# Optimization experiments

Hardware: AMD Instinct MI355X
Metric: run time of the kernel (lower is better)

Reference implementation:

```python
import jax, jax.numpy as jnp
import numpy as np

D_MODEL = 1024
NUM_HEADS = 16
D_K = D_MODEL // NUM_HEADS


def setup_inputs() -> dict:
    key = jax.random.key(0)
    ks = jax.random.split(key, 9)
    s = 1.0 / np.sqrt(D_MODEL)
    x = jax.random.normal(ks[0], (2, 2048, D_MODEL), dtype=jnp.float32)
    Wq = jax.random.uniform(ks[1], (D_MODEL, D_MODEL), jnp.float32, -s, s)
    bq = jax.random.uniform(ks[2], (D_MODEL,), jnp.float32, -s, s)
    Wk = jax.random.uniform(ks[3], (D_MODEL, D_MODEL), jnp.float32, -s, s)
    bk = jax.random.uniform(ks[4], (D_MODEL,), jnp.float32, -s, s)
    Wv = jax.random.uniform(ks[5], (D_MODEL, D_MODEL), jnp.float32, -s, s)
    bv = jax.random.uniform(ks[6], (D_MODEL,), jnp.float32, -s, s)
    Wo = jax.random.uniform(ks[7], (D_MODEL, D_MODEL), jnp.float32, -s, s)
    bo = jax.random.uniform(ks[8], (D_MODEL,), jnp.float32, -s, s)
    return {"x": x, "Wq": Wq, "bq": bq, "Wk": Wk, "bk": bk,
            "Wv": Wv, "bv": bv, "Wo": Wo, "bo": bo}


def reference(x, Wq, bq, Wk, bk, Wv, bv, Wo, bo):
    B, S, _ = x.shape
    # torch Linear: y = x @ W.T + b
    def proj(W, b):
        h = x @ W.T + b                       # [B,S,D]
        return h.reshape(B, S, NUM_HEADS, D_K).transpose(0, 2, 1, 3)  # [B,H,S,Dk]
    Q = proj(Wq, bq)
    K = proj(Wk, bk)
    V = proj(Wv, bv)
    scale = 1.0 / np.sqrt(D_K)
    scores = jnp.einsum('bhqd,bhkd->bhqk', Q, K) * scale   # [B,H,S,S]
    causal = jnp.triu(jnp.ones((S, S), dtype=bool), k=1)   # True above diag
    scores = jnp.where(causal, -jnp.inf, scores)
    probs = jax.nn.softmax(scores, axis=-1)
    out = jnp.einsum('bhqk,bhkd->bhqd', probs, V)          # [B,H,S,Dk]
    out = out.transpose(0, 2, 1, 3).reshape(B, S, NUM_HEADS * D_K)
    return out @ Wo.T + bo
```

## Files before the change

kernel.cpp:

```cpp
#include <hip/hip_runtime.h>

typedef unsigned short u16;
typedef __attribute__((ext_vector_type(8))) short short8;
typedef __attribute__((ext_vector_type(4))) float floatx4;

__device__ __forceinline__ u16 f2bf(float x){
  union { float f; unsigned u; } v; v.f = x;
  unsigned r = v.u + 0x7fffu + ((v.u >> 16) & 1u);
  return (u16)(r >> 16);
}

__device__ __forceinline__ unsigned cvt_pk_bf16(float lo, float hi){
  unsigned r;
  asm("v_cvt_pk_bf16_f32 %0, %1, %2" : "=v"(r) : "v"(lo), "v"(hi));
  return r;
}

__device__ __forceinline__ float exp2_raw(float x){
  float r;
  asm("v_exp_f32 %0, %1" : "=v"(r) : "v"(x));
  return r;
}

__device__ __forceinline__ void gld16(const u16* g, u16* l){
  __builtin_amdgcn_global_load_lds(
      (const __attribute__((address_space(1))) void*)g,
      (__attribute__((address_space(3))) void*)l, 16, 0, 0);
}

#define WAIT_BAR_V4() asm volatile("s_waitcnt vmcnt(4) lgkmcnt(0)\ns_barrier" ::: "memory")
#define WAIT_BAR_V3() asm volatile("s_waitcnt vmcnt(3) lgkmcnt(0)\ns_barrier" ::: "memory")
#define WAIT_BAR_V0() asm volatile("s_waitcnt vmcnt(0) lgkmcnt(0)\ns_barrier" ::: "memory")

__global__ void k_cvt_all(const float* __restrict__ x,
                          const float* __restrict__ wq, const float* __restrict__ wk,
                          const float* __restrict__ wv, const float* __restrict__ wo,
                          u16* __restrict__ xb, u16* __restrict__ wqb, u16* __restrict__ wkb,
                          u16* __restrict__ wvb, u16* __restrict__ wob){
  const int i = blockIdx.x * 256 + threadIdx.x;
  const float* s; u16* d; int off;
  if (i < 1048576) { s = x; d = xb; off = i; }
  else {
    const int j = i - 1048576;
    const int wsel = j >> 18;
    off = j & 262143;
    s = (wsel==0) ? wq : (wsel==1) ? wk : (wsel==2) ? wv : wo;
    d = (wsel==0) ? wqb : (wsel==1) ? wkb : (wsel==2) ? wvb : wob;
  }
  const float4 f = ((const float4*)s)[off];
  unsigned lo = (unsigned)f2bf(f.x) | ((unsigned)f2bf(f.y) << 16);
  unsigned hi = (unsigned)f2bf(f.z) | ((unsigned)f2bf(f.w) << 16);
  ((uint2*)d)[off] = make_uint2(lo, hi);
}

__global__ __launch_bounds__(256) void k_gemm_qkv(
    const u16* __restrict__ A,
    const u16* __restrict__ Wq, const u16* __restrict__ Wk, const u16* __restrict__ Wv,
    const float* __restrict__ bq, const float* __restrict__ bk, const float* __restrict__ bv,
    u16* __restrict__ Qo, u16* __restrict__ Ko, u16* __restrict__ Vo)
{
  const int bid = (int)blockIdx.x;
  const int xcd = bid & 7;
  const int i5  = bid >> 3;
  const int xb_ = ((xcd >> 2) << 2) + (i5 & 3);
  const int rest = i5 >> 2;
  const int yb_ = ((xcd & 3) << 3) + (rest & 7);
  const int mode = rest >> 3;

  const u16* W      = (mode==1) ? Wk : (mode==2) ? Wv : Wq;
  const float* bias = (mode==1) ? bk : (mode==2) ? bv : bq;

  __shared__ u16 lA[3][4096];
  __shared__ u16 lB[3][4096];

  const int tid  = threadIdx.x;
  const int row0 = yb_ * 128;
  const int col0 = xb_ * 128;

  const int srow = tid >> 2;
  const int sgp  = tid & 3;
  const int sgl  = sgp ^ ((srow >> 1) & 3);
  const u16* ga0 = A + (row0 + srow)      * 1024 + sgl * 8;
  const u16* ga1 = A + (row0 + srow + 64) * 1024 + sgl * 8;
  const u16* gb0 = W + (col0 + srow)      * 1024 + sgl * 8;
  const u16* gb1 = W + (col0 + srow + 64) * 1024 + sgl * 8;

  const int l  = tid & 63, w = tid >> 6;
  const int wr = w >> 1,  wc = w & 1;
  const int lr = l & 15,  grp = l >> 4;
  const int sw = (lr >> 1) & 3;
  int aoff[4], boff[4];
#pragma unroll
  for (int m = 0; m < 4; ++m) aoff[m] = (wr*64 + m*16 + lr)*32 + ((grp ^ sw) * 8);
#pragma unroll
  for (int n = 0; n < 4; ++n) boff[n] = (wc*64 + n*16 + lr)*32 + ((grp ^ sw) * 8);

  floatx4 acc[4][4];
#pragma unroll
  for (int m = 0; m < 4; ++m)
#pragma unroll
    for (int n = 0; n < 4; ++n) acc[m][n] = (floatx4){0.f, 0.f, 0.f, 0.f};

#define STAGE(buf, kt_) do { \
    const int k0_ = (kt_) * 32; \
    gld16(ga0 + k0_, &lA[(buf)][tid*8]); \
    gld16(ga1 + k0_, &lA[(buf)][2048 + tid*8]); \
    gld16(gb0 + k0_, &lB[(buf)][tid*8]); \
    gld16(gb1 + k0_, &lB[(buf)][2048 + tid*8]); \
  } while (0)

  STAGE(0, 0);
  STAGE(1, 1);
  asm volatile("s_waitcnt vmcnt(4)\ns_barrier" ::: "memory");

  for (int kt0 = 0; kt0 < 32; kt0 += 3) {
#pragma unroll
    for (int i = 0; i < 3; ++i) {
      const int kt = kt0 + i;
      if (kt >= 32) break;
      const bool st2 = (kt + 2 < 32);
      if (st2) STAGE((i + 2) % 3, kt + 2);
      short8 af[4], bf[4];
#pragma unroll
      for (int m = 0; m < 4; ++m) af[m] = *(const short8*)&lA[i][aoff[m]];
#pragma unroll
      for (int n = 0; n < 4; ++n) bf[n] = *(const short8*)&lB[i][boff[n]];
#pragma unroll
      for (int m = 0; m < 4; ++m)
#pragma unroll
        for (int n = 0; n < 4; ++n)
          acc[m][n] = __builtin_amdgcn_mfma_f32_16x16x32_bf16(af[m], bf[n], acc[m][n], 0, 0, 0);
      if (st2) WAIT_BAR_V4(); else WAIT_BAR_V0();
    }
  }
#undef STAGE

  const float sc = (mode == 0) ? 0.18033688011112042f : 1.0f;
  u16* dst = (mode == 0) ? Qo : (mode == 1) ? Ko : Vo;
#pragma unroll
  for (int n = 0; n < 4; ++n) {
    const int cg = col0 + wc*64 + n*16 + lr;
    const float bb = bias[cg];
    const int h = cg >> 6, d = cg & 63;
#pragma unroll
    for (int m = 0; m < 4; ++m) {
#pragma unroll
      for (int j = 0; j < 4; ++j) {
        const int rg = row0 + wr*64 + m*16 + grp*4 + j;
        const int b = rg >> 11, s5 = rg & 2047;
        const float val = (acc[m][n][j] + bb) * sc;
        int idx;
        if (mode == 2) idx = ((b*16 + h)*64 + d)*2048 + s5;
        else           idx = ((b*16 + h)*2048 + s5)*64 + d;
        dst[idx] = f2bf(val);
      }
    }
  }
}

__global__ __launch_bounds__(256) void k_gemm_o(
    const u16* __restrict__ A, const u16* __restrict__ W,
    const float* __restrict__ bias, float* __restrict__ Fo)
{
  const int bid = (int)blockIdx.x;
  const int xcd = bid & 7;
  const int i5  = bid >> 3;
  const int xb_ = ((xcd >> 2) << 2) + (i5 & 3);
  const int yb_ = ((xcd & 3) << 4) + (i5 >> 2);

  __shared__ u16 lA[3][2048];
  __shared__ u16 lB[3][4096];

  const int tid  = threadIdx.x;
  const int row0 = yb_ * 64;
  const int col0 = xb_ * 128;

  const int srow = tid >> 2;
  const int sgp  = tid & 3;
  const int sgl  = sgp ^ ((srow >> 1) & 3);
  const u16* ga0 = A + (row0 + srow)      * 1024 + sgl * 8;
  const u16* gb0 = W + (col0 + srow)      * 1024 + sgl * 8;
  const u16* gb1 = W + (col0 + srow + 64) * 1024 + sgl * 8;

  const int l  = tid & 63, w = tid >> 6;
  const int wr = w >> 1,  wc = w & 1;
  const int lr = l & 15,  grp = l >> 4;
  const int sw = (lr >> 1) & 3;
  int aoff[2], boff[4];
#pragma unroll
  for (int m = 0; m < 2; ++m) aoff[m] = (wr*32 + m*16 + lr)*32 + ((grp ^ sw) * 8);
#pragma unroll
  for (int n = 0; n < 4; ++n) boff[n] = (wc*64 + n*16 + lr)*32 + ((grp ^ sw) * 8);

  floatx4 acc[2][4];
#pragma unroll
  for (int m = 0; m < 2; ++m)
#pragma unroll
    for (int n = 0; n < 4; ++n) acc[m][n] = (floatx4){0.f, 0.f, 0.f, 0.f};

#define STAGE(buf, kt_) do { \
    const int k0_ = (kt_) * 32; \
    gld16(ga0 + k0_, &lA[(buf)][tid*8]); \
    gld16(gb0 + k0_, &lB[(buf)][tid*8]); \
    gld16(gb1 + k0_, &lB[(buf)][2048 + tid*8]); \
  } while (0)

  STAGE(0, 0);
  STAGE(1, 1);
  asm volatile("s_waitcnt vmcnt(3)\ns_barrier" ::: "memory");

  for (int kt0 = 0; kt0 < 32; kt0 += 3) {
#pragma unroll
    for (int i = 0; i < 3; ++i) {
      const int kt = kt0 + i;
      if (kt >= 32) break;
      const bool st2 = (kt + 2 < 32);
      if (st2) STAGE((i + 2) % 3, kt + 2);
      short8 af[2], bf[4];
#pragma unroll
      for (int m = 0; m < 2; ++m) af[m] = *(const short8*)&lA[i][aoff[m]];
#pragma unroll
      for (int n = 0; n < 4; ++n) bf[n] = *(const short8*)&lB[i][boff[n]];
#pragma unroll
      for (int m = 0; m < 2; ++m)
#pragma unroll
        for (int n = 0; n < 4; ++n)
          acc[m][n] = __builtin_amdgcn_mfma_f32_16x16x32_bf16(af[m], bf[n], acc[m][n], 0, 0, 0);
      if (st2) WAIT_BAR_V3(); else WAIT_BAR_V0();
    }
  }
#undef STAGE

#pragma unroll
  for (int n = 0; n < 4; ++n) {
    const int cg = col0 + wc*64 + n*16 + lr;
    const float bb = bias[cg];
#pragma unroll
    for (int m = 0; m < 2; ++m) {
      const int rg = row0 + wr*32 + m*16 + grp*4;
#pragma unroll
      for (int j = 0; j < 4; ++j)
        Fo[(rg + j) * 1024 + cg] = acc[m][n][j] + bb;
    }
  }
}

__global__ __launch_bounds__(256, 4) void k_attn(
    const u16* __restrict__ Q, const u16* __restrict__ K,
    const u16* __restrict__ V, u16* __restrict__ O)
{
  __shared__ u16 lK[2][4096];
  __shared__ u16 lV[2][4096];
  __shared__ u16 lP[4][1024];

  const int tid = threadIdx.x;
  const int bid = (int)blockIdx.x;
  const int xcd = bid & 7, r = bid >> 3;
  const int k_ = r & 31, j_ = r >> 5;
  const int bh = xcd * 4 + j_;
  const int qt = (j_ & 1) ? k_ : (31 - k_);

  const int l = tid & 63, w = tid >> 6;
  const int lr = l & 15, grp = l >> 4;
  const int qw0 = qt * 64 + w * 16;
  const int nkt = qt + 1;

  const u16* Qh = Q + (size_t)bh * 2048 * 64;
  const u16* Kh = K + (size_t)bh * 2048 * 64;
  const u16* Vh = V + (size_t)bh * 64 * 2048;

  const int srow = tid >> 3, sgp = tid & 7;
  const int sgl = sgp ^ (srow & 7);
  u16* lPw = &lP[w][0];
  const int swz = lr & 7;
  const int b = bh >> 4, h = bh & 15;

#define STAGEKV(buf, kt_) do { \
    gld16(Kh + ((kt_)*64 + srow     )*64 + sgl*8, &lK[(buf)][tid*8]); \
    gld16(Kh + ((kt_)*64 + srow + 32)*64 + sgl*8, &lK[(buf)][2048 + tid*8]); \
    gld16(Vh + (srow     )*2048 + (kt_)*64 + sgl*8, &lV[(buf)][tid*8]); \
    gld16(Vh + (srow + 32)*2048 + (kt_)*64 + sgl*8, &lV[(buf)][2048 + tid*8]); \
  } while (0)

  short8 qf[2];
#pragma unroll
  for (int kk = 0; kk < 2; ++kk)
    qf[kk] = *(const short8*)(Qh + (qw0 + lr)*64 + kk*32 + grp*8);

  floatx4 accO[4];
  float mrow = -1e30f, lrow = 0.f;
#pragma unroll
  for (int dn = 0; dn < 4; ++dn) accO[dn] = (floatx4){0.f, 0.f, 0.f, 0.f};

  STAGEKV(0, 0);
  __syncthreads();

  for (int kt0 = 0; kt0 < nkt; kt0 += 2) {
#pragma unroll
    for (int i = 0; i < 2; ++i) {
      const int kt = kt0 + i;
      if (kt >= nkt) break;
      if (kt + 1 < nkt) STAGEKV(i ^ 1, kt + 1);
      const int kb = kt * 64;

      floatx4 st[4];
#pragma unroll
      for (int n = 0; n < 4; ++n) st[n] = (floatx4){0.f, 0.f, 0.f, 0.f};
#pragma unroll
      for (int n = 0; n < 4; ++n) {
        const int key = n*16 + lr;
#pragma unroll
        for (int kk = 0; kk < 2; ++kk) {
          const int gp = (kk*4 + grp) ^ (key & 7);
          short8 kf = *(const short8*)&lK[i][key*64 + gp*8];
          st[n] = __builtin_amdgcn_mfma_f32_16x16x32_bf16(kf, qf[kk], st[n], 0, 0, 0);
        }
      }

      const int lim = qw0 + lr - kb;
      if (63 > lim) {
#pragma unroll
        for (int n = 0; n < 4; ++n)
#pragma unroll
          for (int jj = 0; jj < 4; ++jj)
            if (n*16 + grp*4 + jj > lim) st[n][jj] = -1e30f;
      }

      float mt = st[0][0];
#pragma unroll
      for (int n = 0; n < 4; ++n)
#pragma unroll
        for (int jj = 0; jj < 4; ++jj) mt = fmaxf(mt, st[n][jj]);
      if (!__all(mt <= mrow + 8.0f)) {
        float mg = fmaxf(mt, __shfl_xor(mt, 16));
        mg = fmaxf(mg, __shfl_xor(mg, 32));
        const float mn = fmaxf(mrow, mg);
        const float alpha = exp2_raw(mrow - mn);
        mrow = mn;
        lrow *= alpha;
#pragma unroll
        for (int dn = 0; dn < 4; ++dn) accO[dn] *= alpha;
      }
      float ps = 0.f;
#pragma unroll
      for (int n = 0; n < 4; ++n)
#pragma unroll
        for (int jj = 0; jj < 4; ++jj) {
          const float p = exp2_raw(st[n][jj] - mrow);
          st[n][jj] = p;
          ps += p;
        }
      lrow += ps;

#pragma unroll
      for (int n = 0; n < 4; ++n)
#pragma unroll
        for (int p2 = 0; p2 < 2; ++p2) {
          const unsigned pk = cvt_pk_bf16(st[n][2*p2], st[n][2*p2+1]);
          const int pg = (2*n + (grp >> 1)) ^ swz;
          ((unsigned*)lPw)[lr*32 + pg*4 + (grp & 1)*2 + p2] = pk;
        }

      asm volatile("s_waitcnt lgkmcnt(0)" ::: "memory");

      short8 pa[2];
#pragma unroll
      for (int kk = 0; kk < 2; ++kk)
        pa[kk] = *(const short8*)&lPw[lr*64 + (((kk*4 + grp) ^ swz) * 8)];

#pragma unroll
      for (int dn = 0; dn < 4; ++dn) {
        const int d = dn*16 + lr;
#pragma unroll
        for (int kk = 0; kk < 2; ++kk) {
          const int gp = (kk*4 + grp) ^ (d & 7);
          short8 vf = *(const short8*)&lV[i][d*64 + gp*8];
          accO[dn] = __builtin_amdgcn_mfma_f32_16x16x32_bf16(vf, pa[kk], accO[dn], 0, 0, 0);
        }
      }
      __syncthreads();
    }
  }

  float lt = lrow + __shfl_xor(lrow, 16);
  lt += __shfl_xor(lt, 32);
  const float inv = 1.0f / lt;
  const int token = b*2048 + qw0 + lr;
#pragma unroll
  for (int dn = 0; dn < 4; ++dn)
#pragma unroll
    for (int p2 = 0; p2 < 2; ++p2) {
      const unsigned pk = cvt_pk_bf16(accO[dn][2*p2] * inv, accO[dn][2*p2+1] * inv);
      *(unsigned*)&O[token*1024 + h*64 + dn*16 + grp*4 + 2*p2] = pk;
    }
#undef STAGEKV
}

extern "C" void kernel_launch(void* const* d_in, const int* in_sizes, int n_in,
                              void* d_out, int out_size, void* d_ws, size_t ws_size,
                              hipStream_t stream) {
  const float* x  = (const float*)d_in[0];
  const float* Wq = (const float*)d_in[1];
  const float* bq = (const float*)d_in[2];
  const float* Wk = (const float*)d_in[3];
  const float* bk = (const float*)d_in[4];
  const float* Wv = (const float*)d_in[5];
  const float* bv = (const float*)d_in[6];
  const float* Wo = (const float*)d_in[7];
  const float* bo = (const float*)d_in[8];
  float* out = (float*)d_out;

  char* ws = (char*)d_ws;
  u16* xb  = (u16*)(ws + 0);
  u16* wqb = (u16*)(ws + 8388608);
  u16* wkb = (u16*)(ws + 10485760);
  u16* wvb = (u16*)(ws + 12582912);
  u16* wob = (u16*)(ws + 14680064);
  u16* Qb  = (u16*)(ws + 16777216);
  u16* Kb  = (u16*)(ws + 25165824);
  u16* Vb  = (u16*)(ws + 33554432);
  u16* Ab  = (u16*)(ws + 41943040);

  k_cvt_all<<<dim3(8192), 256, 0, stream>>>(x, Wq, Wk, Wv, Wo, xb, wqb, wkb, wvb, wob);

  k_gemm_qkv<<<dim3(768), 256, 0, stream>>>(xb, wqb, wkb, wvb, bq, bk, bv, Qb, Kb, Vb);

  k_attn<<<dim3(1024), 256, 0, stream>>>(Qb, Kb, Vb, Ab);

  k_gemm_o<<<dim3(512), 256, 0, stream>>>(Ab, wob, bo, out);
}
```

Baseline: 106.3 us.

## Fuse Q/K/V projections into one block sharing the A tile

```diff
diff --git a/kernel.cpp b/kernel.cpp
--- a/kernel.cpp
+++ b/kernel.cpp
@@ -28,7 +28,6 @@
       (__attribute__((address_space(3))) void*)l, 16, 0, 0);
 }
 
-#define WAIT_BAR_V4() asm volatile("s_waitcnt vmcnt(4) lgkmcnt(0)\ns_barrier" ::: "memory")
 #define WAIT_BAR_V3() asm volatile("s_waitcnt vmcnt(3) lgkmcnt(0)\ns_barrier" ::: "memory")
 #define WAIT_BAR_V0() asm volatile("s_waitcnt vmcnt(0) lgkmcnt(0)\ns_barrier" ::: "memory")
 
@@ -63,15 +62,10 @@
   const int xcd = bid & 7;
   const int i5  = bid >> 3;
   const int xb_ = ((xcd >> 2) << 2) + (i5 & 3);
-  const int rest = i5 >> 2;
-  const int yb_ = ((xcd & 3) << 3) + (rest & 7);
-  const int mode = rest >> 3;
-
-  const u16* W      = (mode==1) ? Wk : (mode==2) ? Wv : Wq;
-  const float* bias = (mode==1) ? bk : (mode==2) ? bv : bq;
-
-  __shared__ u16 lA[3][4096];
-  __shared__ u16 lB[3][4096];
+  const int yb_ = ((xcd & 3) << 3) + (i5 >> 2);
+
+  __shared__ u16 lA[2][4096];
+  __shared__ u16 lW[2][3][4096];
 
   const int tid  = threadIdx.x;
   const int row0 = yb_ * 128;
@@ -80,10 +74,14 @@
   const int srow = tid >> 2;
   const int sgp  = tid & 3;
   const int sgl  = sgp ^ ((srow >> 1) & 3);
-  const u16* ga0 = A + (row0 + srow)      * 1024 + sgl * 8;
-  const u16* ga1 = A + (row0 + srow + 64) * 1024 + sgl * 8;
-  const u16* gb0 = W + (col0 + srow)      * 1024 + sgl * 8;
-  const u16* gb1 = W + (col0 + srow + 64) * 1024 + sgl * 8;
+  const u16* ga0 = A  + (row0 + srow)      * 1024 + sgl * 8;
+  const u16* ga1 = A  + (row0 + srow + 64) * 1024 + sgl * 8;
+  const u16* gq0 = Wq + (col0 + srow)      * 1024 + sgl * 8;
+  const u16* gq1 = Wq + (col0 + srow + 64) * 1024 + sgl * 8;
+  const u16* gk0 = Wk + (col0 + srow)      * 1024 + sgl * 8;
+  const u16* gk1 = Wk + (col0 + srow + 64) * 1024 + sgl * 8;
+  const u16* gv0 = Wv + (col0 + srow)      * 1024 + sgl * 8;
+  const u16* gv1 = Wv + (col0 + srow + 64) * 1024 + sgl * 8;
 
   const int l  = tid & 63, w = tid >> 6;
   const int wr = w >> 1,  wc = w & 1;
@@ -95,64 +93,77 @@
 #pragma unroll
   for (int n = 0; n < 4; ++n) boff[n] = (wc*64 + n*16 + lr)*32 + ((grp ^ sw) * 8);
 
-  floatx4 acc[4][4];
+  floatx4 accQ[4][4], accK[4][4], accV[4][4];
 #pragma unroll
   for (int m = 0; m < 4; ++m)
 #pragma unroll
-    for (int n = 0; n < 4; ++n) acc[m][n] = (floatx4){0.f, 0.f, 0.f, 0.f};
+    for (int n = 0; n < 4; ++n) {
+      accQ[m][n] = (floatx4){0.f, 0.f, 0.f, 0.f};
+      accK[m][n] = (floatx4){0.f, 0.f, 0.f, 0.f};
+      accV[m][n] = (floatx4){0.f, 0.f, 0.f, 0.f};
+    }
 
 #define STAGE(buf, kt_) do { \
     const int k0_ = (kt_) * 32; \
     gld16(ga0 + k0_, &lA[(buf)][tid*8]); \
     gld16(ga1 + k0_, &lA[(buf)][2048 + tid*8]); \
-    gld16(gb0 + k0_, &lB[(buf)][tid*8]); \
-    gld16(gb1 + k0_, &lB[(buf)][2048 + tid*8]); \
+    gld16(gq0 + k0_, &lW[(buf)][0][tid*8]); \
+    gld16(gq1 + k0_, &lW[(buf)][0][2048 + tid*8]); \
+    gld16(gk0 + k0_, &lW[(buf)][1][tid*8]); \
+    gld16(gk1 + k0_, &lW[(buf)][1][2048 + tid*8]); \
+    gld16(gv0 + k0_, &lW[(buf)][2][tid*8]); \
+    gld16(gv1 + k0_, &lW[(buf)][2][2048 + tid*8]); \
   } while (0)
 
   STAGE(0, 0);
-  STAGE(1, 1);
-  asm volatile("s_waitcnt vmcnt(4)\ns_barrier" ::: "memory");
-
-  for (int kt0 = 0; kt0 < 32; kt0 += 3) {
-#pragma unroll
-    for (int i = 0; i < 3; ++i) {
+  asm volatile("s_waitcnt vmcnt(0)\ns_barrier" ::: "memory");
+
+  for (int kt0 = 0; kt0 < 32; kt0 += 2) {
+#pragma unroll
+    for (int i = 0; i < 2; ++i) {
       const int kt = kt0 + i;
-      if (kt >= 32) break;
-      const bool st2 = (kt + 2 < 32);
-      if (st2) STAGE((i + 2) % 3, kt + 2);
-      short8 af[4], bf[4];
+      if (kt + 1 < 32) STAGE(i ^ 1, kt + 1);
+
+      short8 af[4];
 #pragma unroll
       for (int m = 0; m < 4; ++m) af[m] = *(const short8*)&lA[i][aoff[m]];
-#pragma unroll
-      for (int n = 0; n < 4; ++n) bf[n] = *(const short8*)&lB[i][boff[n]];
+
+      short8 bq_[4], bk_[4], bv_[4];
+#pragma unroll
+      for (int n = 0; n < 4; ++n) {
+        bq_[n] = *(const short8*)&lW[i][0][boff[n]];
+        bk_[n] = *(const short8*)&lW[i][1][boff[n]];
+        bv_[n] = *(const short8*)&lW[i][2][boff[n]];
+      }
 #pragma unroll
       for (int m = 0; m < 4; ++m)
 #pragma unroll
-        for (int n = 0; n < 4; ++n)
-          acc[m][n] = __builtin_amdgcn_mfma_f32_16x16x32_bf16(af[m], bf[n], acc[m][n], 0, 0, 0);
-      if (st2) WAIT_BAR_V4(); else WAIT_BAR_V0();
+        for (int n = 0; n < 4; ++n) {
+          accQ[m][n] = __builtin_amdgcn_mfma_f32_16x16x32_bf16(af[m], bq_[n], accQ[m][n], 0, 0, 0);
+          accK[m][n] = __builtin_amdgcn_mfma_f32_16x16x32_bf16(af[m], bk_[n], accK[m][n], 0, 0, 0);
+          accV[m][n] = __builtin_amdgcn_mfma_f32_16x16x32_bf16(af[m], bv_[n], accV[m][n], 0, 0, 0);
+        }
+      WAIT_BAR_V0();
     }
   }
 #undef STAGE
 
-  const float sc = (mode == 0) ? 0.18033688011112042f : 1.0f;
-  u16* dst = (mode == 0) ? Qo : (mode == 1) ? Ko : Vo;
 #pragma unroll
   for (int n = 0; n < 4; ++n) {
     const int cg = col0 + wc*64 + n*16 + lr;
-    const float bb = bias[cg];
     const int h = cg >> 6, d = cg & 63;
+    const float bbq = bq[cg], bbk = bk[cg], bbv = bv[cg];
 #pragma unroll
     for (int m = 0; m < 4; ++m) {
 #pragma unroll
       for (int j = 0; j < 4; ++j) {
         const int rg = row0 + wr*64 + m*16 + grp*4 + j;
         const int b = rg >> 11, s5 = rg & 2047;
-        const float val = (acc[m][n][j] + bb) * sc;
-        int idx;
-        if (mode == 2) idx = ((b*16 + h)*64 + d)*2048 + s5;
-        else           idx = ((b*16 + h)*2048 + s5)*64 + d;
-        dst[idx] = f2bf(val);
+        const int idxQK = ((b*16 + h)*2048 + s5)*64 + d;
+        const int idxV  = ((b*16 + h)*64 + d)*2048 + s5;
+        Qo[idxQK] = f2bf((accQ[m][n][j] + bbq) * 0.18033688011112042f);
+        Ko[idxQK] = f2bf(accK[m][n][j] + bbk);
+        Vo[idxV]  = f2bf(accV[m][n][j] + bbv);
       }
     }
   }
@@ -423,7 +434,7 @@
 
   k_cvt_all<<<dim3(8192), 256, 0, stream>>>(x, Wq, Wk, Wv, Wo, xb, wqb, wkb, wvb, wob);
 
-  k_gemm_qkv<<<dim3(768), 256, 0, stream>>>(xb, wqb, wkb, wvb, bq, bk, bv, Qb, Kb, Vb);
+  k_gemm_qkv<<<dim3(256), 256, 0, stream>>>(xb, wqb, wkb, wvb, bq, bk, bv, Qb, Kb, Vb);
 
   k_attn<<<dim3(1024), 256, 0, stream>>>(Qb, Kb, Vb, Ab);
 
```

Result: slower. 114.0 us (+7.3%).
